# Performance work log

Hardware: AMD Instinct MI355X
Metric: run time of the kernel (lower is better)

Reference implementation:

```python
import math
import jax, jax.numpy as jnp
import numpy as np

B, S, D, H = 4, 2048, 1024, 16
DK = D // H


def setup_inputs() -> dict:
    key = jax.random.key(0)
    kx, kq, kk, kv, ko = jax.random.split(key, 5)
    scale = 1.0 / math.sqrt(D)
    return {
        "x": jax.random.normal(kx, (B, S, D), dtype=jnp.float32),
        "wq": jax.random.normal(kq, (D, D), dtype=jnp.float32) * scale,
        "wk": jax.random.normal(kk, (D, D), dtype=jnp.float32) * scale,
        "wv": jax.random.normal(kv, (D, D), dtype=jnp.float32) * scale,
        "wo": jax.random.normal(ko, (D, D), dtype=jnp.float32) * scale,
    }


def reference(x, wq, wk, wv, wo):
    b, s, d = x.shape
    # projections -> [b, h, s, dk]
    def split_heads(t):
        return t.reshape(b, s, H, DK).transpose(0, 2, 1, 3)
    q = split_heads(x @ wq)
    k = split_heads(x @ wk)
    v = split_heads(x @ wv)
    # scores [b, h, s, s], scaled by sqrt(d_k)
    scores = jnp.einsum('bhqd,bhkd->bhqk', q, k) / math.sqrt(DK)
    causal = jnp.tril(jnp.ones((s, s), dtype=bool))  # [s, s]
    scores = jnp.where(causal[None, None, :, :], scores, -jnp.inf)
    weights = jax.nn.softmax(scores, axis=-1)
    weights = jnp.nan_to_num(weights, nan=0.0)
    attn = jnp.einsum('bhqk,bhkd->bhqd', weights, v)
    attn = attn.transpose(0, 2, 1, 3).reshape(b, s, d)
    return attn @ wo
```

## Files before the change

kernel.cpp:

```cpp
#include <hip/hip_runtime.h>
#include <hip/hip_bf16.h>
#include <math.h>

#define B_ 4
#define S_ 2048
#define D_ 1024
#define H_ 16
#define DK_ 64

typedef __bf16 bf16;
typedef bf16 bf16x8 __attribute__((ext_vector_type(8)));
typedef float f32x4 __attribute__((ext_vector_type(4)));
typedef float f32x16 __attribute__((ext_vector_type(16)));

__device__ __forceinline__ int swz8(int row, int slot) {
    return row * 64 + ((slot ^ (row & 7)) << 3);
}
__device__ __forceinline__ unsigned packbf(float a, float b) {
    union { bf16 h[2]; unsigned u; } x;
    x.h[0] = (bf16)a; x.h[1] = (bf16)b;
    return x.u;
}
__device__ __forceinline__ void permswap(unsigned& x, unsigned& y) {
    asm("v_permlane32_swap_b32 %0, %1" : "+v"(x), "+v"(y));
}
__device__ __forceinline__ float fexp2(float x) {
#if __has_builtin(__builtin_amdgcn_exp2f)
    return __builtin_amdgcn_exp2f(x);
#else
    float r;
    asm("v_exp_f32 %0, %1" : "=v"(r) : "v"(x));
    return r;
#endif
}
__device__ __forceinline__ void gld16(bf16* lbase, const bf16* gsrc) {
    __builtin_amdgcn_global_load_lds(
        (const __attribute__((address_space(1))) unsigned*)gsrc,
        (__attribute__((address_space(3))) unsigned*)lbase, 16, 0, 0);
}

__global__ __launch_bounds__(256) void cast_x_kernel(const float* __restrict__ x, bf16* __restrict__ xb) {
    const size_t i = ((size_t)blockIdx.x * 256 + threadIdx.x) * 8;
    const float4* src = (const float4*)(x + i);
    float4 f0 = src[0], f1 = src[1];
    bf16x8 v;
    v[0] = (bf16)f0.x; v[1] = (bf16)f0.y; v[2] = (bf16)f0.z; v[3] = (bf16)f0.w;
    v[4] = (bf16)f1.x; v[5] = (bf16)f1.y; v[6] = (bf16)f1.z; v[7] = (bf16)f1.w;
    *(bf16x8*)(xb + i) = v;
}

__global__ void transpose_w_kernel(const float* wq, const float* wk, const float* wv, const float* wo,
                                   bf16* wqkvT, bf16* woT) {
    __shared__ float t[32][33];
    const int z = blockIdx.z;
    const float* src = (z == 0) ? wq : (z == 1) ? wk : (z == 2) ? wv : wo;
    bf16* dst = (z < 3) ? (wqkvT + (size_t)z * 1024 * 1024) : woT;
    const int n0 = blockIdx.x * 32, k0 = blockIdx.y * 32;
    const int tx = threadIdx.x, ty = threadIdx.y;
#pragma unroll
    for (int j = 0; j < 4; ++j)
        t[ty + j * 8][tx] = src[(size_t)(k0 + ty + j * 8) * 1024 + n0 + tx];
    __syncthreads();
#pragma unroll
    for (int j = 0; j < 4; ++j)
        dst[(size_t)(n0 + ty + j * 8) * 1024 + k0 + tx] = (bf16)t[tx][ty + j * 8];
}

template <int MODE>
__global__ __launch_bounds__(256) void gemm_kernel(const bf16* __restrict__ A, const bf16* __restrict__ Bt,
                                                   void* o0, void* o1, void* o2,
                                                   int M, int N, int K, int NT) {
    __shared__ __align__(16) bf16 As[128 * 64];
    __shared__ __align__(16) bf16 Bs[128 * 64];
    const int tid = threadIdx.x;
    const int lane = tid & 63;
    const int w = tid >> 6;
    const int wm = w >> 1, wn = w & 1;
    const int g = lane >> 4, r16 = lane & 15;

    const int bid = blockIdx.x;
    const int qch = gridDim.x >> 3;
    const int wg = (bid & 7) * qch + (bid >> 3);
    const int mt = wg / NT, nt = wg % NT;
    const int m0 = mt * 128, n0 = nt * 128;

    const int srow = tid >> 3;
    const int sslot = (tid & 7) ^ (srow & 7);
    const bf16* ga = A + (size_t)(m0 + srow) * K + sslot * 8;
    const bf16* gb = Bt + (size_t)(n0 + srow) * K + sslot * 8;

    f32x4 acc[4][4] = {};

    for (int kt = 0; kt < K; kt += 64) {
#pragma unroll
        for (int p = 0; p < 4; ++p) {
            gld16(&As[p * 2048 + w * 512], ga + (size_t)p * 32 * K + kt);
            gld16(&Bs[p * 2048 + w * 512], gb + (size_t)p * 32 * K + kt);
        }
        __syncthreads();
#pragma unroll
        for (int k0 = 0; k0 < 2; ++k0) {
            bf16x8 af[4], bfr[4];
#pragma unroll
            for (int mf = 0; mf < 4; ++mf)
                af[mf] = *(const bf16x8*)&As[swz8(wm * 64 + mf * 16 + r16, 4 * k0 + g)];
#pragma unroll
            for (int nf = 0; nf < 4; ++nf)
                bfr[nf] = *(const bf16x8*)&Bs[swz8(wn * 64 + nf * 16 + r16, 4 * k0 + g)];
#pragma unroll
            for (int mf = 0; mf < 4; ++mf)
#pragma unroll
                for (int nf = 0; nf < 4; ++nf)
                    acc[mf][nf] = __builtin_amdgcn_mfma_f32_16x16x32_bf16(af[mf], bfr[nf], acc[mf][nf], 0, 0, 0);
        }
        __syncthreads();
    }

    if (MODE == 0) {
        const int seg = nt >> 3;
#pragma unroll
        for (int mf = 0; mf < 4; ++mf) {
#pragma unroll
            for (int nf = 0; nf < 4; ++nf) {
                const int col = n0 + wn * 64 + nf * 16 + r16;
                const int n1 = col & 1023;
                const int h = n1 >> 6, dk = n1 & 63;
                const int row0 = m0 + wm * 64 + mf * 16 + 4 * g;
                const int b = row0 >> 11, s0 = row0 & 2047;
                if (seg == 2) {
                    union { bf16 h4[4]; unsigned long long u; } pk;
#pragma unroll
                    for (int rr = 0; rr < 4; ++rr) pk.h4[rr] = (bf16)acc[mf][nf][rr];
                    *(unsigned long long*)((bf16*)o2 + (((size_t)b * H_ + h) * DK_ + dk) * S_ + s0) = pk.u;
                } else {
                    bf16* dst = (seg == 0) ? (bf16*)o0 : (bf16*)o1;
#pragma unroll
                    for (int rr = 0; rr < 4; ++rr)
                        dst[(((size_t)b * H_ + h) * S_ + s0 + rr) * DK_ + dk] = (bf16)acc[mf][nf][rr];
                }
            }
        }
    } else {
#pragma unroll
        for (int mf = 0; mf < 4; ++mf)
#pragma unroll
            for (int nf = 0; nf < 4; ++nf)
#pragma unroll
                for (int rr = 0; rr < 4; ++rr) {
                    int row = m0 + wm * 64 + mf * 16 + 4 * g + rr;
                    int col = n0 + wn * 64 + nf * 16 + r16;
                    ((float*)o0)[(size_t)row * N + col] = acc[mf][nf][rr];
                }
    }
}

__global__ __launch_bounds__(256, 4) void attn_kernel(const bf16* __restrict__ Q,
                                                      const bf16* __restrict__ Kb,
                                                      const bf16* __restrict__ Vt,
                                                      bf16* __restrict__ ctx) {
    __shared__ __align__(16) bf16 lds[4][4096];
    const int bh = blockIdx.x;
    const int qt = 15 - (int)blockIdx.y;
    const int tid = threadIdx.x;
    const int lane = tid & 63, w = tid >> 6;
    const int lq = lane & 31, hi = lane >> 5;
    const int q0 = qt * 128;
    const int q0w = q0 + w * 32;
    const int q = q0w + lq;
    const int njt = 2 * qt + 2;
    const float qscale = 0.125f * 1.44269504088896340736f;

    const int srow = tid >> 3;
    const int sslot = (tid & 7) ^ (srow & 7);
    const bf16* kg = Kb + ((size_t)bh * S_ + srow) * DK_ + sslot * 8;
    const bf16* vg = Vt + ((size_t)bh * DK_ + srow) * S_ + sslot * 8;

    bf16x8 qf[4];
    {
        const bf16* qp = Q + ((size_t)bh * S_ + q) * DK_ + hi * 8;
#pragma unroll
        for (int kc = 0; kc < 4; ++kc) {
            bf16x8 raw = *(const bf16x8*)(qp + kc * 16);
#pragma unroll
            for (int e = 0; e < 8; ++e) qf[kc][e] = (bf16)((float)raw[e] * qscale);
        }
    }

    f32x16 accd[2] = {};
    float lsum = 0.f;

    bf16x8 kreg0 = *(const bf16x8*)kg;
    bf16x8 kreg1 = *(const bf16x8*)(kg + 32 * DK_);
    bf16x8 vreg0 = *(const bf16x8*)vg;
    bf16x8 vreg1 = *(const bf16x8*)(vg + 32 * S_);

    for (int jt = 0; jt < njt; ++jt) {
        const int cur = jt & 1;
        *(bf16x8*)&lds[cur][tid * 8] = kreg0;
        *(bf16x8*)&lds[cur][tid * 8 + 2048] = kreg1;
        *(bf16x8*)&lds[2 + cur][tid * 8] = vreg0;
        *(bf16x8*)&lds[2 + cur][tid * 8 + 2048] = vreg1;
        if (jt + 1 < njt) {
            kreg0 = *(const bf16x8*)(kg + (size_t)(jt + 1) * 64 * DK_);
            kreg1 = *(const bf16x8*)(kg + (size_t)(jt + 1) * 64 * DK_ + 32 * DK_);
            vreg0 = *(const bf16x8*)(vg + (jt + 1) * 64);
            vreg1 = *(const bf16x8*)(vg + (jt + 1) * 64 + 32 * S_);
        }
        __syncthreads();

        if (jt * 64 <= q0w + 31) {
            f32x16 sacc[2];
#pragma unroll
            for (int c = 0; c < 2; ++c)
#pragma unroll
                for (int r = 0; r < 16; ++r) sacc[c][r] = -16.0f;
            __builtin_amdgcn_s_setprio(1);
#pragma unroll
            for (int kc = 0; kc < 4; ++kc) {
#pragma unroll
                for (int c = 0; c < 2; ++c) {
                    bf16x8 kf = *(const bf16x8*)&lds[cur][swz8(c * 32 + lq, kc * 2 + hi)];
                    sacc[c] = __builtin_amdgcn_mfma_f32_32x32x16_bf16(kf, qf[kc], sacc[c], 0, 0, 0);
                }
            }
            __builtin_amdgcn_s_setprio(0);

            if (jt * 64 + 63 > q0w) {
#pragma unroll
                for (int c = 0; c < 2; ++c)
#pragma unroll
                    for (int r = 0; r < 16; ++r) {
                        int key = jt * 64 + c * 32 + (r & 3) + 8 * (r >> 2) + 4 * hi;
                        if (key > q) sacc[c][r] = -INFINITY;
                    }
            }

#pragma unroll
            for (int c = 0; c < 2; ++c)
#pragma unroll
                for (int r = 0; r < 16; ++r) sacc[c][r] = fexp2(sacc[c][r]);

            float s8[8];
#pragma unroll
            for (int i = 0; i < 8; ++i)
                s8[i] = (sacc[0][i] + sacc[0][i + 8]) + (sacc[1][i] + sacc[1][i + 8]);
#pragma unroll
            for (int i = 0; i < 4; ++i) s8[i] += s8[i + 4];
            lsum += (s8[0] + s8[1]) + (s8[2] + s8[3]);

#pragma unroll
            for (int kc = 0; kc < 4; ++kc) {
                const int c = kc >> 1, kf2 = kc & 1;
                unsigned w0 = packbf(sacc[c][8 * kf2 + 0], sacc[c][8 * kf2 + 1]);
                unsigned w1 = packbf(sacc[c][8 * kf2 + 2], sacc[c][8 * kf2 + 3]);
                unsigned w2 = packbf(sacc[c][8 * kf2 + 4], sacc[c][8 * kf2 + 5]);
                unsigned w3 = packbf(sacc[c][8 * kf2 + 6], sacc[c][8 * kf2 + 7]);
                permswap(w0, w2);
                permswap(w1, w3);
                union { unsigned wd[4]; bf16x8 v; } u;
                u.wd[0] = w0; u.wd[1] = w1; u.wd[2] = w2; u.wd[3] = w3;
                __builtin_amdgcn_s_setprio(1);
#pragma unroll
                for (int dt = 0; dt < 2; ++dt) {
                    bf16x8 vf = *(const bf16x8*)&lds[2 + cur][swz8(dt * 32 + lq, kc * 2 + hi)];
                    accd[dt] = __builtin_amdgcn_mfma_f32_32x32x16_bf16(vf, u.v, accd[dt], 0, 0, 0);
                }
                __builtin_amdgcn_s_setprio(0);
            }
        }
    }

    __syncthreads();
    bf16* eb = &lds[0][0];
    const float rl = 1.0f / (lsum + __shfl_xor(lsum, 32));
    {
        const int rowb = (w * 32 + lq) * 128;
        const int rsw = (lq & 7) << 4;
#pragma unroll
        for (int dt = 0; dt < 2; ++dt)
#pragma unroll
            for (int rq = 0; rq < 4; ++rq) {
                union { bf16 h[4]; unsigned long long u64; } pk;
#pragma unroll
                for (int j = 0; j < 4; ++j) pk.h[j] = (bf16)(accd[dt][rq * 4 + j] * rl);
                int off = rowb + ((dt * 64 + rq * 16 + hi * 8) ^ rsw);
                *(unsigned long long*)((char*)eb + off) = pk.u64;
            }
    }
    __syncthreads();
    {
        const int row = tid >> 1, half = tid & 1;
        const int b = bh >> 4, h = bh & 15;
        bf16* op = ctx + ((size_t)b * S_ + q0 + row) * D_ + h * DK_ + half * 32;
#pragma unroll
        for (int i = 0; i < 4; ++i) {
            int sl = half * 4 + i;
            int sls = sl ^ (row & 7);
            bf16x8 v = *(const bf16x8*)((const char*)eb + row * 128 + sls * 16);
            *(bf16x8*)(op + i * 8) = v;
        }
    }
}

extern "C" void kernel_launch(void* const* d_in, const int* in_sizes, int n_in,
                              void* d_out, int out_size, void* d_ws, size_t ws_size,
                              hipStream_t stream) {
    const float* x  = (const float*)d_in[0];
    const float* wq = (const float*)d_in[1];
    const float* wk = (const float*)d_in[2];
    const float* wv = (const float*)d_in[3];
    const float* wo = (const float*)d_in[4];

    char* ws = (char*)d_ws;
    bf16* wqkvT = (bf16*)(ws);
    bf16* woT   = (bf16*)(ws + 6291456);
    bf16* Qb    = (bf16*)(ws + 8388608);
    bf16* Kb    = (bf16*)(ws + 25165824);
    bf16* Vtb   = (bf16*)(ws + 58720256);
    bf16* ctx   = (bf16*)(ws + 75497472);
    bf16* xb    = ctx;

    cast_x_kernel<<<4096, 256, 0, stream>>>(x, xb);
    transpose_w_kernel<<<dim3(32, 32, 4), dim3(32, 8), 0, stream>>>(wq, wk, wv, wo, wqkvT, woT);
    gemm_kernel<0><<<1536, 256, 0, stream>>>(xb, wqkvT, Qb, Kb, Vtb, 8192, 3072, 1024, 24);
    attn_kernel<<<dim3(64, 16), 256, 0, stream>>>(Qb, Kb, Vtb, ctx);
    gemm_kernel<1><<<512, 256, 0, stream>>>(ctx, woT, d_out, nullptr, nullptr, 8192, 1024, 1024, 8);
}
```

Measured before the change: 158.9 us.

## Use 256x256 double-buffered tiles with 512 threads for QKV projection GEMM

Replaces the templated 128x128 GEMM for the QKV projection with a dedicated kernel that uses 256x256 output tiles, 8 waves, and a two-stage LDS double buffer fed by direct global-to-LDS loads with explicit vmcnt waits and barriers. Larger tiles raise arithmetic intensity per loaded byte, and prefetching two stages ahead overlaps global loads with MFMA work. The output GEMM is split into its own non-templated kernel and is otherwise unchanged. The trade-offs are heavier register and LDS use (128KB LDS per block, 128 accumulator floats per thread) and only 384 blocks, which may limit occupancy and tail balance.

Result: slower. 163.5 us (+2.9%).

```diff
diff --git a/kernel.cpp b/kernel.cpp
--- a/kernel.cpp
+++ b/kernel.cpp
@@ -66,10 +66,124 @@
         dst[(size_t)(n0 + ty + j * 8) * 1024 + k0 + tx] = (bf16)t[tx][ty + j * 8];
 }
 
-template <int MODE>
-__global__ __launch_bounds__(256) void gemm_kernel(const bf16* __restrict__ A, const bf16* __restrict__ Bt,
-                                                   void* o0, void* o1, void* o2,
-                                                   int M, int N, int K, int NT) {
+__global__ __launch_bounds__(512, 2) void gemm_qkv_kernel(const bf16* __restrict__ A, const bf16* __restrict__ Bt,
+                                                          bf16* __restrict__ Qb, bf16* __restrict__ Kb,
+                                                          bf16* __restrict__ Vt) {
+    __shared__ __align__(16) bf16 lds[2][32768];
+    const int tid = threadIdx.x;
+    const int lane = tid & 63;
+    const int w = tid >> 6;
+    const int wm = w >> 2, wn = w & 3;
+    const int g = lane >> 4, r16 = lane & 15;
+
+    const int bid = blockIdx.x;
+    const int wg = (bid & 7) * 48 + (bid >> 3);
+    const int mt = wg / 12, ntile = wg % 12;
+    const int m0 = mt * 256, n0 = ntile * 256;
+
+    const int srow = tid >> 3;
+    const int sslot = (tid & 7) ^ (srow & 7);
+    const bf16* ga = A + (size_t)(m0 + srow) * 1024 + sslot * 8;
+    const bf16* gb = Bt + (size_t)(n0 + srow) * 1024 + sslot * 8;
+    const int wbase = w * 512;
+
+    f32x4 acc[8][4] = {};
+
+    auto STAGE = [&](int buf, int t) {
+        bf16* As = &lds[buf][0];
+        bf16* Bs = &lds[buf][16384];
+        const int kt = t * 64;
+#pragma unroll
+        for (int p = 0; p < 4; ++p)
+            gld16(&As[p * 4096 + wbase], ga + (size_t)p * 65536 + kt);
+#pragma unroll
+        for (int p = 0; p < 4; ++p)
+            gld16(&Bs[p * 4096 + wbase], gb + (size_t)p * 65536 + kt);
+    };
+
+    STAGE(0, 0);
+    STAGE(1, 1);
+    asm volatile("s_waitcnt vmcnt(8)" ::: "memory");
+    __builtin_amdgcn_sched_barrier(0);
+    __builtin_amdgcn_s_barrier();
+    __builtin_amdgcn_sched_barrier(0);
+
+    for (int t = 0; t < 16; ++t) {
+        const bf16* As = &lds[t & 1][0];
+        const bf16* Bs = &lds[t & 1][16384];
+        __builtin_amdgcn_s_setprio(1);
+#pragma unroll
+        for (int mh = 0; mh < 2; ++mh) {
+            bf16x8 af[4][2];
+#pragma unroll
+            for (int mf = 0; mf < 4; ++mf)
+#pragma unroll
+                for (int k0 = 0; k0 < 2; ++k0)
+                    af[mf][k0] = *(const bf16x8*)&As[swz8(wm * 128 + mh * 64 + mf * 16 + r16, 4 * k0 + g)];
+#pragma unroll
+            for (int nh = 0; nh < 2; ++nh) {
+                bf16x8 bfr[2][2];
+#pragma unroll
+                for (int nf = 0; nf < 2; ++nf)
+#pragma unroll
+                    for (int k0 = 0; k0 < 2; ++k0)
+                        bfr[nf][k0] = *(const bf16x8*)&Bs[swz8(wn * 64 + nh * 32 + nf * 16 + r16, 4 * k0 + g)];
+#pragma unroll
+                for (int k0 = 0; k0 < 2; ++k0)
+#pragma unroll
+                    for (int mf = 0; mf < 4; ++mf)
+#pragma unroll
+                        for (int nf = 0; nf < 2; ++nf)
+                            acc[mh * 4 + mf][nh * 2 + nf] = __builtin_amdgcn_mfma_f32_16x16x32_bf16(
+                                af[mf][k0], bfr[nf][k0], acc[mh * 4 + mf][nh * 2 + nf], 0, 0, 0);
+            }
+        }
+        __builtin_amdgcn_s_setprio(0);
+        __builtin_amdgcn_sched_barrier(0);
+        __builtin_amdgcn_s_barrier();
+        __builtin_amdgcn_sched_barrier(0);
+        if (t + 2 < 16) {
+            STAGE(t & 1, t + 2);
+            asm volatile("s_waitcnt vmcnt(8)" ::: "memory");
+        } else {
+            asm volatile("s_waitcnt vmcnt(0)" ::: "memory");
+        }
+        __builtin_amdgcn_sched_barrier(0);
+        __builtin_amdgcn_s_barrier();
+        __builtin_amdgcn_sched_barrier(0);
+    }
+
+    const int seg = ntile >> 2;
+#pragma unroll
+    for (int mh = 0; mh < 2; ++mh) {
+#pragma unroll
+        for (int mf = 0; mf < 4; ++mf) {
+#pragma unroll
+            for (int nq = 0; nq < 4; ++nq) {
+                const int col = n0 + wn * 64 + nq * 16 + r16;
+                const int n1 = col & 1023;
+                const int h = n1 >> 6, dk = n1 & 63;
+                const int row0 = m0 + wm * 128 + mh * 64 + mf * 16 + 4 * g;
+                const int b = row0 >> 11, s0 = row0 & 2047;
+                f32x4 v = acc[mh * 4 + mf][nq];
+                if (seg == 2) {
+                    union { bf16 h4[4]; unsigned long long u; } pk;
+#pragma unroll
+                    for (int rr = 0; rr < 4; ++rr) pk.h4[rr] = (bf16)v[rr];
+                    *(unsigned long long*)(Vt + (((size_t)b * H_ + h) * DK_ + dk) * S_ + s0) = pk.u;
+                } else {
+                    bf16* dst = (seg == 0) ? Qb : Kb;
+#pragma unroll
+                    for (int rr = 0; rr < 4; ++rr)
+                        dst[(((size_t)b * H_ + h) * S_ + s0 + rr) * DK_ + dk] = (bf16)v[rr];
+                }
+            }
+        }
+    }
+}
+
+__global__ __launch_bounds__(256) void gemm_out_kernel(const bf16* __restrict__ A, const bf16* __restrict__ Bt,
+                                                       float* __restrict__ o0, int M, int N, int K, int NT) {
     __shared__ __align__(16) bf16 As[128 * 64];
     __shared__ __align__(16) bf16 Bs[128 * 64];
     const int tid = threadIdx.x;
@@ -116,42 +230,16 @@
         __syncthreads();
     }
 
-    if (MODE == 0) {
-        const int seg = nt >> 3;
-#pragma unroll
-        for (int mf = 0; mf < 4; ++mf) {
-#pragma unroll
-            for (int nf = 0; nf < 4; ++nf) {
-                const int col = n0 + wn * 64 + nf * 16 + r16;
-                const int n1 = col & 1023;
-                const int h = n1 >> 6, dk = n1 & 63;
-                const int row0 = m0 + wm * 64 + mf * 16 + 4 * g;
-                const int b = row0 >> 11, s0 = row0 & 2047;
-                if (seg == 2) {
-                    union { bf16 h4[4]; unsigned long long u; } pk;
-#pragma unroll
-                    for (int rr = 0; rr < 4; ++rr) pk.h4[rr] = (bf16)acc[mf][nf][rr];
-                    *(unsigned long long*)((bf16*)o2 + (((size_t)b * H_ + h) * DK_ + dk) * S_ + s0) = pk.u;
-                } else {
-                    bf16* dst = (seg == 0) ? (bf16*)o0 : (bf16*)o1;
-#pragma unroll
-                    for (int rr = 0; rr < 4; ++rr)
-                        dst[(((size_t)b * H_ + h) * S_ + s0 + rr) * DK_ + dk] = (bf16)acc[mf][nf][rr];
-                }
-            }
-        }
-    } else {
-#pragma unroll
-        for (int mf = 0; mf < 4; ++mf)
-#pragma unroll
-            for (int nf = 0; nf < 4; ++nf)
-#pragma unroll
-                for (int rr = 0; rr < 4; ++rr) {
-                    int row = m0 + wm * 64 + mf * 16 + 4 * g + rr;
-                    int col = n0 + wn * 64 + nf * 16 + r16;
-                    ((float*)o0)[(size_t)row * N + col] = acc[mf][nf][rr];
-                }
-    }
+#pragma unroll
+    for (int mf = 0; mf < 4; ++mf)
+#pragma unroll
+        for (int nf = 0; nf < 4; ++nf)
+#pragma unroll
+            for (int rr = 0; rr < 4; ++rr) {
+                int row = m0 + wm * 64 + mf * 16 + 4 * g + rr;
+                int col = n0 + wn * 64 + nf * 16 + r16;
+                o0[(size_t)row * N + col] = acc[mf][nf][rr];
+            }
 }
 
 __global__ __launch_bounds__(256, 4) void attn_kernel(const bf16* __restrict__ Q,
@@ -322,7 +410,7 @@
 
     cast_x_kernel<<<4096, 256, 0, stream>>>(x, xb);
     transpose_w_kernel<<<dim3(32, 32, 4), dim3(32, 8), 0, stream>>>(wq, wk, wv, wo, wqkvT, woT);
-    gemm_kernel<0><<<1536, 256, 0, stream>>>(xb, wqkvT, Qb, Kb, Vtb, 8192, 3072, 1024, 24);
+    gemm_qkv_kernel<<<384, 512, 0, stream>>>(xb, wqkvT, Qb, Kb, Vtb);
     attn_kernel<<<dim3(64, 16), 256, 0, stream>>>(Qb, Kb, Vtb, ctx);
-    gemm_kernel<1><<<512, 256, 0, stream>>>(ctx, woT, d_out, nullptr, nullptr, 8192, 1024, 1024, 8);
-}
+    gemm_out_kernel<<<512, 256, 0, stream>>>(ctx, woT, (float*)d_out, 8192, 1024, 1024, 8);
+}
```
